# Kernel optimization log

Measured on AMD Instinct MI355X. Metric: run time of the kernel, lower is better.

Reference implementation:

```python
import jax, jax.numpy as jnp
import numpy as np

B, N, K = 4, 2048, 32
H, DS, DE = 128, 128, 128
NUM_IN = DS + DE + H  # 384
SCALE = 30.0
EPS = 1e-5


def setup_inputs() -> dict:
    key = jax.random.key(0)
    ks = jax.random.split(key, 9)
    s = 0.05
    return {
        "h_S": jax.random.normal(ks[0], (B, N, DS), jnp.float32),
        "h_V": jax.random.normal(ks[1], (B, N, H), jnp.float32),
        "h_E": jax.random.normal(ks[2], (B, N, K, DE), jnp.float32),
        "E_idx": jax.random.randint(ks[3], (B, N, K), 0, N, jnp.int64),
        "mask_attend": jnp.ones((B, N, K), jnp.float32),
        "W1_w": jax.random.normal(ks[4], (H + NUM_IN, H), jnp.float32) * s,
        "W1_b": jnp.zeros((H,), jnp.float32),
        "W2_w": jax.random.normal(ks[5], (H, H), jnp.float32) * s,
        "W2_b": jnp.zeros((H,), jnp.float32),
        "ln_g": jnp.ones((H,), jnp.float32),
        "ln_b": jnp.zeros((H,), jnp.float32),
    }


def gather_nodes(nodes, idx):
    # nodes: [B, N, D], idx: [B, N, K] -> [B, N, K, D]
    b, n, k = idx.shape
    d = nodes.shape[-1]
    flat = jnp.broadcast_to(idx.reshape(b, n * k, 1), (b, n * k, d))
    return jnp.take_along_axis(nodes, flat, axis=1).reshape(b, n, k, d)


def layer_norm(x, g, b):
    mu = jnp.mean(x, axis=-1, keepdims=True)
    var = jnp.var(x, axis=-1, keepdims=True)
    return (x - mu) * jax.lax.rsqrt(var + EPS) * g + b


def reference(h_S, h_V, h_E, E_idx, mask_attend, W1_w, W1_b, W2_w, W2_b, ln_g, ln_b):
    # h_ES = cat(h_E, gather(h_S))  -> [B,N,K,DE+DS]
    h_ES = jnp.concatenate([h_E, gather_nodes(h_S, E_idx)], axis=-1)
    # h_EXV = cat(h_ES, gather(h_V)) -> [B,N,K,DE+DS+H], masked
    h_EXV = jnp.concatenate([h_ES, gather_nodes(h_V, E_idx)], axis=-1)
    h_EXV = mask_attend[..., None] * h_EXV
    # h_EV = cat(h_V expanded, h_EXV) -> [B,N,K,H+NUM_IN]
    h_V_exp = jnp.broadcast_to(h_V[:, :, None, :], (h_V.shape[0], h_V.shape[1], K, h_V.shape[2]))
    h_EV = jnp.concatenate([h_V_exp, h_EXV], axis=-1)
    # per-edge 2-layer MLP (exact GELU as torch.nn.GELU)
    h = jax.nn.gelu(jnp.einsum("bnkf,fh->bnkh", h_EV, W1_w) + W1_b, approximate=False)
    h_message = jnp.einsum("bnkh,hg->bnkg", h, W2_w) + W2_b
    dh = jnp.sum(h_message, axis=-2) / SCALE
    # dropout is identity in eval mode
    return layer_norm(h_V + dh, ln_g, ln_b)
```

## Files before the change

kernel.cpp:

```cpp
#include <hip/hip_runtime.h>
#include <math.h>

typedef float f32x4 __attribute__((ext_vector_type(4)));
typedef short s16x8 __attribute__((ext_vector_type(8)));
typedef unsigned u32x4 __attribute__((ext_vector_type(4)));

#define N_NODES 2048
#define KEDGE 32
#define HDIM 128
#define SB() __builtin_amdgcn_sched_barrier(0)

__device__ __forceinline__ short f2bf(float f){
  unsigned u = __builtin_bit_cast(unsigned, f);
  u += 0x7fffu + ((u >> 16) & 1u);
  return (short)(u >> 16);
}
__device__ __forceinline__ float bf2f(short s){
  unsigned u = ((unsigned)(unsigned short)s) << 16;
  return __builtin_bit_cast(float, u);
}
__device__ __forceinline__ unsigned cvt_pk_bf16(float a, float b){
  unsigned r;
  asm("v_cvt_pk_bf16_f32 %0, %1, %2" : "=v"(r) : "v"(a), "v"(b));
  return r;
}
__device__ __forceinline__ float fast_gelu(float x){
  float t = x * (-2.3022078f - 0.1029527f * x * x);
  float e = __builtin_amdgcn_exp2f(t);
  return x * __builtin_amdgcn_rcpf(1.0f + e);
}
__device__ __forceinline__ void gld16(const void* g, void* l){
  __builtin_amdgcn_global_load_lds(
      (const __attribute__((address_space(1))) void*)g,
      (__attribute__((address_space(3))) void*)l, 16, 0, 0);
}
__device__ __forceinline__ f32x4 mfma16(s16x8 a, s16x8 b, f32x4 c){
  return __builtin_amdgcn_mfma_f32_16x16x32_bf16(a, b, c, 0, 0, 0);
}

__global__ void prep1(const float* __restrict__ W1, const float* __restrict__ W2,
                      short* __restrict__ W1f, short* __restrict__ W2f,
                      unsigned* __restrict__ flag){
  if (blockIdx.x == 320){
    if (threadIdx.x == 0) *flag = 0u;
    return;
  }
  int t = blockIdx.x * 256 + threadIdx.x;
  if (t < 65536){
    int ks = t >> 12, r = t & 4095;
    int ct = r >> 9;  r &= 511;
    int lane = r >> 3, j = r & 7;
    int k = ks*32 + (lane>>4)*8 + j;
    int n = ct*16 + (lane&15);
    W1f[t] = f2bf(W1[k*128 + n]);
  } else if (t < 81920){
    int t2 = t - 65536;
    int ks = t2 >> 12, r = t2 & 4095;
    int ct = r >> 9;  r &= 511;
    int lane = r >> 3, j = r & 7;
    int k = ks*32 + (lane>>4)*8 + j;
    int n = ct*16 + (lane&15);
    W2f[t2] = f2bf(W2[k*128 + n]);
  }
}

__global__ __launch_bounds__(256)
void prep2(const float* __restrict__ hS, const float* __restrict__ hV,
           const float* __restrict__ b1, const short* __restrict__ W1f,
           short* __restrict__ Zb, unsigned* __restrict__ UHb,
           const unsigned* __restrict__ Ei_u, unsigned* __restrict__ flag){
  if (blockIdx.x >= 128){
    int t = ((int)blockIdx.x - 128)*256 + threadIdx.x;
    unsigned v = Ei_u[2*t + 1];
    unsigned long long m = __ballot(v != 0u);
    if ((threadIdx.x & 63) == 0 && m) atomicOr(flag, 1u);
    return;
  }
  const int tid = threadIdx.x;
  const int w = tid >> 6, lane = tid & 63, l15 = lane & 15, lg = lane >> 4;
  const int nb = ((int)blockIdx.x*4 + w)*16;

  f32x4 accz[8], accu[8];
  #pragma unroll
  for (int ct = 0; ct < 8; ++ct){ accz[ct] = (f32x4){0,0,0,0}; accu[ct] = (f32x4){0,0,0,0}; }

  #pragma unroll
  for (int ks = 0; ks < 4; ++ks){
    const float* p = hS + (long)(nb + l15)*128 + ks*32 + lg*8;
    float4 x = *(const float4*)p, y = *(const float4*)(p + 4);
    u32x4 pk;
    pk[0] = cvt_pk_bf16(x.x, x.y); pk[1] = cvt_pk_bf16(x.z, x.w);
    pk[2] = cvt_pk_bf16(y.x, y.y); pk[3] = cvt_pk_bf16(y.z, y.w);
    s16x8 a = __builtin_bit_cast(s16x8, pk);
    #pragma unroll
    for (int ct = 0; ct < 8; ++ct){
      s16x8 bf = *(const s16x8*)(W1f + (8+ks)*4096 + ct*512 + lane*8);
      accz[ct] = mfma16(a, bf, accz[ct]);
    }
  }
  #pragma unroll
  for (int ks = 0; ks < 4; ++ks){
    const float* p = hV + (long)(nb + l15)*128 + ks*32 + lg*8;
    float4 x = *(const float4*)p, y = *(const float4*)(p + 4);
    u32x4 pk;
    pk[0] = cvt_pk_bf16(x.x, x.y); pk[1] = cvt_pk_bf16(x.z, x.w);
    pk[2] = cvt_pk_bf16(y.x, y.y); pk[3] = cvt_pk_bf16(y.z, y.w);
    s16x8 a = __builtin_bit_cast(s16x8, pk);
    #pragma unroll
    for (int ct = 0; ct < 8; ++ct){
      s16x8 bfd = *(const s16x8*)(W1f + (12+ks)*4096 + ct*512 + lane*8);
      accz[ct] = mfma16(a, bfd, accz[ct]);
      s16x8 bfa = *(const s16x8*)(W1f + (0+ks)*4096 + ct*512 + lane*8);
      accu[ct] = mfma16(a, bfa, accu[ct]);
    }
  }

  float b1v[8];
  #pragma unroll
  for (int ct = 0; ct < 8; ++ct) b1v[ct] = b1[ct*16 + l15];

  #pragma unroll
  for (int ct = 0; ct < 8; ++ct)
    #pragma unroll
    for (int i = 0; i < 4; ++i){
      const long row = nb + lg*4 + i;
      Zb[row*128 + ct*16 + l15] = f2bf(accz[ct][i]);
      unsigned u16 = (unsigned)(unsigned short)f2bf(accu[ct][i] + b1v[ct]);
      unsigned h16 = (unsigned)(unsigned short)f2bf(hV[row*128 + ct*16 + l15]);
      UHb[row*128 + l15*8 + ct] = u16 | (h16 << 16);
    }
}

__global__ __launch_bounds__(256, 1)
void fusedF(const float* __restrict__ hE, const int* __restrict__ Eidx,
            const float* __restrict__ mask,
            const float* __restrict__ W2b, const float* __restrict__ lng,
            const float* __restrict__ lnb, const short* __restrict__ W1f,
            const short* __restrict__ W2f, const short* __restrict__ Zb,
            const unsigned* __restrict__ UHb, const unsigned* __restrict__ idx_flag,
            float* __restrict__ out)
{
  __shared__ __align__(16) char smem[132096];

  const int tid  = threadIdx.x;
  const int w    = tid >> 6;
  const int lane = tid & 63;
  const int l15  = lane & 15;
  const int lg   = lane >> 4;

  const int n0 = ((int)blockIdx.x * 4 + w) * 8;
  const long zrow0 = (long)(n0 >> 11) * N_NODES;

  char* mybuf = smem + w*24576;
  char* W2L   = smem + 98304;
  short* vl   = (short*)(smem + 131072 + w*256);

  unsigned pre[8];
  #pragma unroll
  for (int q = 0; q < 8; ++q){
    const int r = 2*q + (lane >> 5);
    pre[q] = (unsigned)(r*512 + (((lane & 31)*16) ^ ((r & 7) << 4)));
  }

  s16x8 wf[4][8];
  #pragma unroll
  for (int ks = 0; ks < 4; ++ks)
    #pragma unroll
    for (int ct = 0; ct < 8; ++ct)
      wf[ks][ct] = *(const s16x8*)(W1f + (4+ks)*4096 + ct*512 + lane*8);

  #pragma unroll
  for (int q = 0; q < 8; ++q)
    gld16((const char*)W2f + (w*8+q)*1024 + lane*16, W2L + (w*8+q)*1024);

  float w2b8[8], lngv[2], lnbv[2];
  #pragma unroll
  for (int ct = 0; ct < 8; ++ct) w2b8[ct] = W2b[ct*16 + l15];
  #pragma unroll
  for (int q = 0; q < 2; ++q){
    const int c = (lg*2 + q)*16 + l15;
    lngv[q] = lng[c]; lnbv[q] = lnb[c];
  }

  s16x8 ifr[2];
  #pragma unroll
  for (int c2 = 0; c2 < 2; ++c2){
    const int active = ((lg >> 1) == c2);
    const int j = l15 - 8*(lg & 1);
    s16x8 f;
    #pragma unroll
    for (int e = 0; e < 8; ++e)
      f[e] = (active && j == e) ? (short)0x3F80 : (short)0;
    ifr[c2] = f;
  }

  const int is64 = (*idx_flag == 0u);

  #pragma unroll
  for (int hf = 0; hf < 2; ++hf){
    const size_t eb = (size_t)(n0 + (hf>>1))*16384 + (size_t)(hf&1)*8192;
    #pragma unroll
    for (int q = 0; q < 8; ++q)
      gld16((const char*)hE + eb + pre[q], mybuf + hf*8192 + q*1024);
  }

  float maskC, maskN1, maskN2;
  s16x8 uhC[2], uhN1[2], uhN2[2];
  s16x8 zbC[4], zbN1[4], zbN2[4];
  int eN2, eN3;
  {
    const int e0i = n0*32 + 0*16 + l15;
    const int e1i = n0*32 + 1*16 + l15;
    const int e2i = (n0+1)*32 + 0*16 + l15;
    const int ea = is64 ? Eidx[2*e0i] : Eidx[e0i];
    const int eb = is64 ? Eidx[2*e1i] : Eidx[e1i];
    eN2 = is64 ? Eidx[2*e2i] : Eidx[e2i];
    maskC  = mask[e0i];
    maskN1 = mask[e1i];
    #pragma unroll
    for (int ks = 0; ks < 4; ++ks){
      zbC[ks]  = *(const s16x8*)(Zb + (zrow0 + ea)*128 + ks*32 + lg*8);
      zbN1[ks] = *(const s16x8*)(Zb + (zrow0 + eb)*128 + ks*32 + lg*8);
    }
    uhC[0]  = *(const s16x8*)((const short*)UHb + (long)n0*256 + l15*16);
    uhC[1]  = *(const s16x8*)((const short*)UHb + (long)n0*256 + l15*16 + 8);
    uhN1[0] = uhC[0]; uhN1[1] = uhC[1];
  }

  asm volatile("s_waitcnt vmcnt(0)" ::: "memory");
  SB();
  __builtin_amdgcn_s_barrier();

  float vacc[8];
  #pragma unroll
  for (int ct = 0; ct < 8; ++ct) vacc[ct] = 0.f;

  int cs = 0;

  #pragma unroll 2
  for (int it = 0; it < 16; ++it){
    const int hfA = (it + 2) & 15;
    const int hfE = (it + 3) & 15;
    const int nA  = n0 + (hfA >> 1);
    SB();
    maskN2 = mask[nA*32 + (hfA&1)*16 + l15];
    uhN2[0] = *(const s16x8*)((const short*)UHb + (long)nA*256 + l15*16);
    uhN2[1] = *(const s16x8*)((const short*)UHb + (long)nA*256 + l15*16 + 8);
    {
      const int eE = (n0 + (hfE>>1))*32 + (hfE&1)*16 + l15;
      eN3 = is64 ? Eidx[2*eE] : Eidx[eE];
    }
    SB();
    {
      const int ss = (cs >= 1) ? cs - 1 : 2;
      char* sbuf = mybuf + ss*8192;
      const size_t eb = (size_t)nA*16384 + (size_t)(hfA&1)*8192;
      #pragma unroll
      for (int q = 0; q < 8; ++q)
        gld16((const char*)hE + eb + pre[q], sbuf + q*1024);
    }
    SB();
    #pragma unroll
    for (int ks = 0; ks < 4; ++ks)
      zbN2[ks] = *(const s16x8*)(Zb + (zrow0 + eN2)*128 + ks*32 + lg*8);
    SB();
    asm volatile("s_waitcnt vmcnt(34)" ::: "memory");
    SB();

    f32x4 acc1[8];
    #pragma unroll
    for (int ct = 0; ct < 8; ++ct) acc1[ct] = (f32x4){0,0,0,0};

    const char* cbuf = mybuf + cs*8192;
    const int sw = (l15 & 7) << 4;
    const int rowb = l15 * 512;
    #pragma unroll
    for (int ks = 0; ks < 4; ++ks){
      const int c0 = ks*128 + lg*32;
      float4 ex = *(const float4*)(cbuf + rowb + (c0 ^ sw));
      float4 ey = *(const float4*)(cbuf + rowb + ((c0 + 16) ^ sw));
      u32x4 pk;
      pk[0] = cvt_pk_bf16(ex.x, ex.y); pk[1] = cvt_pk_bf16(ex.z, ex.w);
      pk[2] = cvt_pk_bf16(ey.x, ey.y); pk[3] = cvt_pk_bf16(ey.z, ey.w);
      s16x8 a = __builtin_bit_cast(s16x8, pk);
      #pragma unroll
      for (int ct = 0; ct < 8; ++ct)
        acc1[ct] = mfma16(a, wf[ks][ct], acc1[ct]);
      #pragma unroll
      for (int c2 = 0; c2 < 2; ++c2)
        acc1[ks*2 + c2] = mfma16(zbC[ks], ifr[c2], acc1[ks*2 + c2]);
    }

    float uv[8];
    #pragma unroll
    for (int ct = 0; ct < 4; ++ct){ uv[ct] = bf2f(uhC[0][2*ct]); uv[4+ct] = bf2f(uhC[1][2*ct]); }
    float mi[4];
    #pragma unroll
    for (int i = 0; i < 4; ++i) mi[i] = __shfl(maskC, lg*4 + i, 64);
    #pragma unroll
    for (int ct = 0; ct < 8; ++ct)
      #pragma unroll
      for (int i = 0; i < 4; ++i)
        vacc[ct] += fast_gelu(uv[ct] + mi[i]*acc1[ct][i]);

    if (it & 1){
      float v8[8];
      #pragma unroll
      for (int ct = 0; ct < 8; ++ct){
        float s = vacc[ct];
        s += __shfl_xor(s, 16, 64);
        s += __shfl_xor(s, 32, 64);
        v8[ct] = s;
        vacc[ct] = 0.f;
      }
      #pragma unroll
      for (int q = 0; q < 2; ++q){
        const int ct = lg*2 + q;
        vl[ct*16 + l15] = f2bf(v8[ct]);
      }
      asm volatile("s_waitcnt lgkmcnt(0)" ::: "memory");
      SB();

      f32x4 acc2[8];
      #pragma unroll
      for (int ct = 0; ct < 8; ++ct) acc2[ct] = (f32x4){0,0,0,0};
      #pragma unroll
      for (int ks2 = 0; ks2 < 4; ++ks2){
        s16x8 av = *(const s16x8*)((const short*)vl + ks2*32 + lg*8);
        const char* wb2 = W2L + ks2*8192 + lane*16;
        #pragma unroll
        for (int ct = 0; ct < 8; ++ct){
          s16x8 bf = *(const s16x8*)(wb2 + ct*1024);
          acc2[ct] = mfma16(av, bf, acc2[ct]);
        }
      }

      float hv[8];
      #pragma unroll
      for (int ct = 0; ct < 4; ++ct){ hv[ct] = bf2f(uhC[0][2*ct+1]); hv[4+ct] = bf2f(uhC[1][2*ct+1]); }
      float res[8], vs = 0.f, vq = 0.f;
      #pragma unroll
      for (int ct = 0; ct < 8; ++ct){
        float dh  = (acc2[ct][0] + 32.0f * w2b8[ct]) * (1.0f/30.0f);
        float val = hv[ct] + dh;
        res[ct] = val;
        vs += val; vq += val*val;
      }
      vs += __shfl_xor(vs, 1, 64);  vs += __shfl_xor(vs, 2, 64);
      vs += __shfl_xor(vs, 4, 64);  vs += __shfl_xor(vs, 8, 64);
      vq += __shfl_xor(vq, 1, 64);  vq += __shfl_xor(vq, 2, 64);
      vq += __shfl_xor(vq, 4, 64);  vq += __shfl_xor(vq, 8, 64);
      const float mu  = vs * (1.0f/128.0f);
      const float var = vq * (1.0f/128.0f) - mu*mu;
      const float rs  = rsqrtf(var + 1e-5f);

      const long nodeoff = (long)(n0 + (it >> 1)) * HDIM;
      #pragma unroll
      for (int q = 0; q < 2; ++q){
        const int ct = lg*2 + q;
        out[nodeoff + ct*16 + l15] = (res[ct] - mu) * rs * lngv[q] + lnbv[q];
      }
    }

    maskC = maskN1; maskN1 = maskN2;
    uhC[0] = uhN1[0]; uhC[1] = uhN1[1];
    uhN1[0] = uhN2[0]; uhN1[1] = uhN2[1];
    #pragma unroll
    for (int ks = 0; ks < 4; ++ks){ zbC[ks] = zbN1[ks]; zbN1[ks] = zbN2[ks]; }
    eN2 = eN3;
    cs = (cs == 2) ? 0 : cs + 1;
    SB();
  }
}

extern "C" void kernel_launch(void* const* d_in, const int* in_sizes, int n_in,
                              void* d_out, int out_size, void* d_ws, size_t ws_size,
                              hipStream_t stream) {
  const float* hS  = (const float*)d_in[0];
  const float* hV  = (const float*)d_in[1];
  const float* hE  = (const float*)d_in[2];
  const int*   Ei  = (const int*)d_in[3];
  const float* mk  = (const float*)d_in[4];
  const float* W1w = (const float*)d_in[5];
  const float* W1b = (const float*)d_in[6];
  const float* W2w = (const float*)d_in[7];
  const float* W2b = (const float*)d_in[8];
  const float* lng = (const float*)d_in[9];
  const float* lnb = (const float*)d_in[10];

  short* W1f = (short*)d_ws;
  short* W2f = W1f + 65536;
  unsigned* flag = (unsigned*)((char*)d_ws + 163840);
  short* Zb = (short*)((char*)d_ws + 164096);
  unsigned* UHb = (unsigned*)((char*)d_ws + 2261248);

  prep1<<<321, 256, 0, stream>>>(W1w, W2w, W1f, W2f, flag);
  prep2<<<640, 256, 0, stream>>>(hS, hV, W1b, W1f, Zb, UHb, (const unsigned*)Ei, flag);
  fusedF<<<256, 256, 0, stream>>>(hE, Ei, mk, W2b, lng, lnb,
                                  W1f, W2f, Zb, UHb, flag, (float*)d_out);
}
```

Before: 94.27 us.

## Split W2+LayerNorm into separate pass and double wave count in fused edge kernel

Moves the second linear layer, bias, residual and LayerNorm out of the fused edge kernel into a new pass3 kernel that reads per-node bf16 sums from workspace. The fused kernel now runs 512 threads per block with 4 nodes per wave, a 2-stage LDS ring instead of 3, and no W2 staging in LDS. Ub no longer packs hV alongside. The aim is more waves in flight to hide hE loading latency, at the cost of an extra kernel launch and a global round trip for the intermediate.

```diff
diff --git a/kernel.cpp b/kernel.cpp
--- a/kernel.cpp
+++ b/kernel.cpp
@@ -67,7 +67,7 @@
 __global__ __launch_bounds__(256)
 void prep2(const float* __restrict__ hS, const float* __restrict__ hV,
            const float* __restrict__ b1, const short* __restrict__ W1f,
-           short* __restrict__ Zb, unsigned* __restrict__ UHb,
+           short* __restrict__ Zb, short* __restrict__ Ub,
            const unsigned* __restrict__ Ei_u, unsigned* __restrict__ flag){
   if (blockIdx.x >= 128){
     int t = ((int)blockIdx.x - 128)*256 + threadIdx.x;
@@ -125,22 +125,17 @@
     for (int i = 0; i < 4; ++i){
       const long row = nb + lg*4 + i;
       Zb[row*128 + ct*16 + l15] = f2bf(accz[ct][i]);
-      unsigned u16 = (unsigned)(unsigned short)f2bf(accu[ct][i] + b1v[ct]);
-      unsigned h16 = (unsigned)(unsigned short)f2bf(hV[row*128 + ct*16 + l15]);
-      UHb[row*128 + l15*8 + ct] = u16 | (h16 << 16);
-    }
-}
-
-__global__ __launch_bounds__(256, 1)
+      Ub[row*128 + l15*8 + ct]  = f2bf(accu[ct][i] + b1v[ct]);
+    }
+}
+
+__global__ __launch_bounds__(512, 2)
 void fusedF(const float* __restrict__ hE, const int* __restrict__ Eidx,
-            const float* __restrict__ mask,
-            const float* __restrict__ W2b, const float* __restrict__ lng,
-            const float* __restrict__ lnb, const short* __restrict__ W1f,
-            const short* __restrict__ W2f, const short* __restrict__ Zb,
-            const unsigned* __restrict__ UHb, const unsigned* __restrict__ idx_flag,
-            float* __restrict__ out)
+            const float* __restrict__ mask, const short* __restrict__ W1f,
+            const short* __restrict__ Zb, const short* __restrict__ Ub,
+            const unsigned* __restrict__ idx_flag, short* __restrict__ vb)
 {
-  __shared__ __align__(16) char smem[132096];
+  __shared__ __align__(16) char smem[131072];
 
   const int tid  = threadIdx.x;
   const int w    = tid >> 6;
@@ -148,12 +143,9 @@
   const int l15  = lane & 15;
   const int lg   = lane >> 4;
 
-  const int n0 = ((int)blockIdx.x * 4 + w) * 8;
+  const int n0 = ((int)blockIdx.x * 8 + w) * 4;
   const long zrow0 = (long)(n0 >> 11) * N_NODES;
-
-  char* mybuf = smem + w*24576;
-  char* W2L   = smem + 98304;
-  short* vl   = (short*)(smem + 131072 + w*256);
+  char* mybuf = smem + w*16384;
 
   unsigned pre[8];
   #pragma unroll
@@ -168,19 +160,7 @@
     #pragma unroll
     for (int ct = 0; ct < 8; ++ct)
       wf[ks][ct] = *(const s16x8*)(W1f + (4+ks)*4096 + ct*512 + lane*8);
-
-  #pragma unroll
-  for (int q = 0; q < 8; ++q)
-    gld16((const char*)W2f + (w*8+q)*1024 + lane*16, W2L + (w*8+q)*1024);
-
-  float w2b8[8], lngv[2], lnbv[2];
-  #pragma unroll
-  for (int ct = 0; ct < 8; ++ct) w2b8[ct] = W2b[ct*16 + l15];
-  #pragma unroll
-  for (int q = 0; q < 2; ++q){
-    const int c = (lg*2 + q)*16 + l15;
-    lngv[q] = lng[c]; lnbv[q] = lnb[c];
-  }
+  SB();
 
   s16x8 ifr[2];
   #pragma unroll
@@ -196,82 +176,66 @@
 
   const int is64 = (*idx_flag == 0u);
 
-  #pragma unroll
-  for (int hf = 0; hf < 2; ++hf){
-    const size_t eb = (size_t)(n0 + (hf>>1))*16384 + (size_t)(hf&1)*8192;
-    #pragma unroll
-    for (int q = 0; q < 8; ++q)
-      gld16((const char*)hE + eb + pre[q], mybuf + hf*8192 + q*1024);
-  }
-
-  float maskC, maskN1, maskN2;
-  s16x8 uhC[2], uhN1[2], uhN2[2];
-  s16x8 zbC[4], zbN1[4], zbN2[4];
-  int eN2, eN3;
+  int e0, eZ;
   {
-    const int e0i = n0*32 + 0*16 + l15;
-    const int e1i = n0*32 + 1*16 + l15;
-    const int e2i = (n0+1)*32 + 0*16 + l15;
-    const int ea = is64 ? Eidx[2*e0i] : Eidx[e0i];
-    const int eb = is64 ? Eidx[2*e1i] : Eidx[e1i];
-    eN2 = is64 ? Eidx[2*e2i] : Eidx[e2i];
-    maskC  = mask[e0i];
-    maskN1 = mask[e1i];
-    #pragma unroll
-    for (int ks = 0; ks < 4; ++ks){
-      zbC[ks]  = *(const s16x8*)(Zb + (zrow0 + ea)*128 + ks*32 + lg*8);
-      zbN1[ks] = *(const s16x8*)(Zb + (zrow0 + eb)*128 + ks*32 + lg*8);
-    }
-    uhC[0]  = *(const s16x8*)((const short*)UHb + (long)n0*256 + l15*16);
-    uhC[1]  = *(const s16x8*)((const short*)UHb + (long)n0*256 + l15*16 + 8);
-    uhN1[0] = uhC[0]; uhN1[1] = uhC[1];
-  }
-
-  asm volatile("s_waitcnt vmcnt(0)" ::: "memory");
+    const int ea = n0*32 + l15;
+    const int eb = n0*32 + 16 + l15;
+    e0 = is64 ? Eidx[2*ea] : Eidx[ea];
+    eZ = is64 ? Eidx[2*eb] : Eidx[eb];
+  }
+  float maskC = mask[n0*32 + l15];
+  s16x8 ubC = *(const s16x8*)(Ub + (long)n0*128 + l15*8);
   SB();
-  __builtin_amdgcn_s_barrier();
+  #pragma unroll
+  for (int q = 0; q < 8; ++q)
+    gld16((const char*)hE + (size_t)n0*16384 + pre[q], mybuf + q*1024);
+  SB();
+  s16x8 zbC[4];
+  #pragma unroll
+  for (int ks = 0; ks < 4; ++ks)
+    zbC[ks] = *(const s16x8*)(Zb + (zrow0 + e0)*128 + ks*32 + lg*8);
+  SB();
 
   float vacc[8];
   #pragma unroll
   for (int ct = 0; ct < 8; ++ct) vacc[ct] = 0.f;
 
-  int cs = 0;
-
-  #pragma unroll 2
-  for (int it = 0; it < 16; ++it){
-    const int hfA = (it + 2) & 15;
-    const int hfE = (it + 3) & 15;
-    const int nA  = n0 + (hfA >> 1);
-    SB();
-    maskN2 = mask[nA*32 + (hfA&1)*16 + l15];
-    uhN2[0] = *(const s16x8*)((const short*)UHb + (long)nA*256 + l15*16);
-    uhN2[1] = *(const s16x8*)((const short*)UHb + (long)nA*256 + l15*16 + 8);
+  #pragma unroll
+  for (int t = 0; t < 8; ++t){
+    const int tn = (t+1) & 7;
+    const int t2 = (t+2) & 7;
+    const int nn_n = n0 + (tn >> 1);
+    SB();
+    float maskN = mask[nn_n*32 + (tn&1)*16 + l15];
+    s16x8 ubN = *(const s16x8*)(Ub + (long)nn_n*128 + l15*8);
+    int eN;
     {
-      const int eE = (n0 + (hfE>>1))*32 + (hfE&1)*16 + l15;
-      eN3 = is64 ? Eidx[2*eE] : Eidx[eE];
+      const int e = (n0 + (t2>>1))*32 + (t2&1)*16 + l15;
+      eN = is64 ? Eidx[2*e] : Eidx[e];
     }
     SB();
     {
-      const int ss = (cs >= 1) ? cs - 1 : 2;
-      char* sbuf = mybuf + ss*8192;
-      const size_t eb = (size_t)nA*16384 + (size_t)(hfA&1)*8192;
+      const size_t eb = (size_t)nn_n*16384 + (size_t)(tn&1)*8192;
+      char* sbuf = mybuf + (tn&1)*8192;
       #pragma unroll
       for (int q = 0; q < 8; ++q)
         gld16((const char*)hE + eb + pre[q], sbuf + q*1024);
     }
     SB();
+    s16x8 zbN[4];
     #pragma unroll
     for (int ks = 0; ks < 4; ++ks)
-      zbN2[ks] = *(const s16x8*)(Zb + (zrow0 + eN2)*128 + ks*32 + lg*8);
-    SB();
-    asm volatile("s_waitcnt vmcnt(34)" ::: "memory");
+      zbN[ks] = *(const s16x8*)(Zb + (zrow0 + eZ)*128 + ks*32 + lg*8);
+    SB();
+    if (t == 0 || (t & 1)) asm volatile("s_waitcnt vmcnt(15)" ::: "memory");
+    else                   asm volatile("s_waitcnt vmcnt(23)" ::: "memory");
     SB();
 
     f32x4 acc1[8];
     #pragma unroll
     for (int ct = 0; ct < 8; ++ct) acc1[ct] = (f32x4){0,0,0,0};
 
-    const char* cbuf = mybuf + cs*8192;
+    const char* cbuf = mybuf + (t&1)*8192;
     const int sw = (l15 & 7) << 4;
     const int rowb = l15 * 512;
     #pragma unroll
@@ -293,7 +257,7 @@
 
     float uv[8];
     #pragma unroll
-    for (int ct = 0; ct < 4; ++ct){ uv[ct] = bf2f(uhC[0][2*ct]); uv[4+ct] = bf2f(uhC[1][2*ct]); }
+    for (int ct = 0; ct < 8; ++ct) uv[ct] = bf2f(ubC[ct]);
     float mi[4];
     #pragma unroll
     for (int i = 0; i < 4; ++i) mi[i] = __shfl(maskC, lg*4 + i, 64);
@@ -303,7 +267,8 @@
       for (int i = 0; i < 4; ++i)
         vacc[ct] += fast_gelu(uv[ct] + mi[i]*acc1[ct][i]);
 
-    if (it & 1){
+    if (t & 1){
+      const long nn = n0 + (t >> 1);
       float v8[8];
       #pragma unroll
       for (int ct = 0; ct < 8; ++ct){
@@ -313,63 +278,69 @@
         v8[ct] = s;
         vacc[ct] = 0.f;
       }
-      #pragma unroll
-      for (int q = 0; q < 2; ++q){
-        const int ct = lg*2 + q;
-        vl[ct*16 + l15] = f2bf(v8[ct]);
+      if (lg == 0){
+        #pragma unroll
+        for (int ct = 0; ct < 8; ++ct)
+          vb[nn*128 + ct*16 + l15] = f2bf(v8[ct]);
       }
-      asm volatile("s_waitcnt lgkmcnt(0)" ::: "memory");
-      SB();
-
-      f32x4 acc2[8];
-      #pragma unroll
-      for (int ct = 0; ct < 8; ++ct) acc2[ct] = (f32x4){0,0,0,0};
-      #pragma unroll
-      for (int ks2 = 0; ks2 < 4; ++ks2){
-        s16x8 av = *(const s16x8*)((const short*)vl + ks2*32 + lg*8);
-        const char* wb2 = W2L + ks2*8192 + lane*16;
-        #pragma unroll
-        for (int ct = 0; ct < 8; ++ct){
-          s16x8 bf = *(const s16x8*)(wb2 + ct*1024);
-          acc2[ct] = mfma16(av, bf, acc2[ct]);
-        }
-      }
-
-      float hv[8];
-      #pragma unroll
-      for (int ct = 0; ct < 4; ++ct){ hv[ct] = bf2f(uhC[0][2*ct+1]); hv[4+ct] = bf2f(uhC[1][2*ct+1]); }
-      float res[8], vs = 0.f, vq = 0.f;
-      #pragma unroll
-      for (int ct = 0; ct < 8; ++ct){
-        float dh  = (acc2[ct][0] + 32.0f * w2b8[ct]) * (1.0f/30.0f);
-        float val = hv[ct] + dh;
-        res[ct] = val;
-        vs += val; vq += val*val;
-      }
-      vs += __shfl_xor(vs, 1, 64);  vs += __shfl_xor(vs, 2, 64);
-      vs += __shfl_xor(vs, 4, 64);  vs += __shfl_xor(vs, 8, 64);
-      vq += __shfl_xor(vq, 1, 64);  vq += __shfl_xor(vq, 2, 64);
-      vq += __shfl_xor(vq, 4, 64);  vq += __shfl_xor(vq, 8, 64);
-      const float mu  = vs * (1.0f/128.0f);
-      const float var = vq * (1.0f/128.0f) - mu*mu;
-      const float rs  = rsqrtf(var + 1e-5f);
-
-      const long nodeoff = (long)(n0 + (it >> 1)) * HDIM;
-      #pragma unroll
-      for (int q = 0; q < 2; ++q){
-        const int ct = lg*2 + q;
-        out[nodeoff + ct*16 + l15] = (res[ct] - mu) * rs * lngv[q] + lnbv[q];
-      }
-    }
-
-    maskC = maskN1; maskN1 = maskN2;
-    uhC[0] = uhN1[0]; uhC[1] = uhN1[1];
-    uhN1[0] = uhN2[0]; uhN1[1] = uhN2[1];
-    #pragma unroll
-    for (int ks = 0; ks < 4; ++ks){ zbC[ks] = zbN1[ks]; zbN1[ks] = zbN2[ks]; }
-    eN2 = eN3;
-    cs = (cs == 2) ? 0 : cs + 1;
-    SB();
+    }
+
+    maskC = maskN; ubC = ubN; eZ = eN;
+    #pragma unroll
+    for (int ks = 0; ks < 4; ++ks) zbC[ks] = zbN[ks];
+  }
+}
+
+__global__ __launch_bounds__(256, 4)
+void pass3(const short* __restrict__ vb, const float* __restrict__ hV,
+           const short* __restrict__ W2f, const float* __restrict__ W2b,
+           const float* __restrict__ lng, const float* __restrict__ lnb,
+           float* __restrict__ out)
+{
+  const int tid = threadIdx.x;
+  const int w = tid >> 6, lane = tid & 63, l15 = lane & 15, lg = lane >> 4;
+  const long m = (long)blockIdx.x*4 + w;
+
+  s16x8 av[4];
+  #pragma unroll
+  for (int ks2 = 0; ks2 < 4; ++ks2)
+    av[ks2] = *(const s16x8*)(vb + m*128 + ks2*32 + lg*8);
+
+  f32x4 acc2[8];
+  #pragma unroll
+  for (int ct = 0; ct < 8; ++ct) acc2[ct] = (f32x4){0,0,0,0};
+  #pragma unroll
+  for (int ks2 = 0; ks2 < 4; ++ks2){
+    const short* wb = W2f + ks2*4096 + lane*8;
+    #pragma unroll
+    for (int ct = 0; ct < 8; ++ct){
+      s16x8 bf = *(const s16x8*)(wb + ct*512);
+      acc2[ct] = mfma16(av[ks2], bf, acc2[ct]);
+    }
+  }
+
+  float res[8], vs = 0.f, vq = 0.f;
+  #pragma unroll
+  for (int ct = 0; ct < 8; ++ct){
+    const int c = ct*16 + l15;
+    float dh  = (acc2[ct][0] + 32.0f * W2b[c]) * (1.0f/30.0f);
+    float val = hV[m*128 + c] + dh;
+    res[ct] = val;
+    vs += val; vq += val*val;
+  }
+  vs += __shfl_xor(vs, 1, 64);  vs += __shfl_xor(vs, 2, 64);
+  vs += __shfl_xor(vs, 4, 64);  vs += __shfl_xor(vs, 8, 64);
+  vq += __shfl_xor(vq, 1, 64);  vq += __shfl_xor(vq, 2, 64);
+  vq += __shfl_xor(vq, 4, 64);  vq += __shfl_xor(vq, 8, 64);
+  const float mu  = vs * (1.0f/128.0f);
+  const float var = vq * (1.0f/128.0f) - mu*mu;
+  const float rs  = rsqrtf(var + 1e-5f);
+
+  #pragma unroll
+  for (int q = 0; q < 2; ++q){
+    const int ct = lg*2 + q;
+    const int c  = ct*16 + l15;
+    out[m*128 + c] = (res[ct] - mu) * rs * lng[c] + lnb[c];
   }
 }
 
@@ -392,10 +363,11 @@
   short* W2f = W1f + 65536;
   unsigned* flag = (unsigned*)((char*)d_ws + 163840);
   short* Zb = (short*)((char*)d_ws + 164096);
-  unsigned* UHb = (unsigned*)((char*)d_ws + 2261248);
+  short* Ub = (short*)((char*)d_ws + 2261248);
+  short* vb = (short*)((char*)d_ws + 4358400);
 
   prep1<<<321, 256, 0, stream>>>(W1w, W2w, W1f, W2f, flag);
-  prep2<<<640, 256, 0, stream>>>(hS, hV, W1b, W1f, Zb, UHb, (const unsigned*)Ei, flag);
-  fusedF<<<256, 256, 0, stream>>>(hE, Ei, mk, W2b, lng, lnb,
-                                  W1f, W2f, Zb, UHb, flag, (float*)d_out);
-}
+  prep2<<<640, 256, 0, stream>>>(hS, hV, W1b, W1f, Zb, Ub, (const unsigned*)Ei, flag);
+  fusedF<<<256, 512, 0, stream>>>(hE, Ei, mk, W1f, Zb, Ub, flag, vb);
+  pass3<<<2048, 256, 0, stream>>>(vb, hV, W2f, W2b, lng, lnb, (float*)d_out);
+}
```

Result: slower. 166.3 us (+76.4%).
